# Optimization experiments

Hardware: AMD Instinct MI355X
Metric: run time of the kernel (lower is better)

Reference implementation:

```python
import jax, jax.numpy as jnp
import numpy as np

B, D, P, E = 256, 512, 128, 128  # batch, in_dim, nproto, projection_dim

def setup_inputs() -> dict:
    key = jax.random.key(0)
    k1, k2 = jax.random.split(key)
    x = jax.random.normal(k1, (B, D, P), dtype=jnp.float32)
    # glorot-uniform-like weights, one [D,E] matrix per prototype
    limit = jnp.sqrt(6.0 / (D + E)).astype(jnp.float32)
    W = jax.random.uniform(k2, (P, D, E), dtype=jnp.float32, minval=-limit, maxval=limit)
    b = jnp.zeros((P, E), dtype=jnp.float32)  # bias per prototype
    return {"x": x, "W": W, "b": b}

def reference(x, W, b):
    # Original: for each proto p, x[:,:,p] @ W_p + b_p, stacked on axis=2.
    # Fused as a single batched GEMM over the prototype axis.
    # x: [B,D,P], W: [P,D,E] -> out: [B,E,P]
    out = jnp.einsum('bdp,pde->bep', x, W)
    out = out + b.T[None, :, :]  # b: [P,E] -> broadcast [1,E,P]
    return out
```

## Files before the change

### kernel.cpp

```cpp
#include <hip/hip_runtime.h>
#include <cstdint>
#include <cstddef>

#define B_ 256
#define D_ 512
#define P_ 128
#define E_ 128

typedef unsigned short u16;
typedef unsigned int   u32;
typedef __bf16  bf16x8_t __attribute__((ext_vector_type(8)));
typedef float   f32x4_t  __attribute__((ext_vector_type(4)));
typedef u16     u16x8_t  __attribute__((ext_vector_type(8)));

__device__ __forceinline__ u16 f2bf(float f) {
  union { float f; unsigned int u; } c; c.f = f;
  unsigned int u = c.u;
  unsigned int r = (u + 0x7FFFu + ((u >> 16) & 1u)) >> 16;
  return (u16)r;
}

__global__ __launch_bounds__(256) void transpose_cvt_kernel(
    const float* __restrict__ src, u16* __restrict__ dst,
    size_t dst_row_stride, size_t dst_outer_stride) {
  __shared__ float tile[64][65];

  const int o  = blockIdx.x;
  const int r0 = blockIdx.y * 64;
  const int c0 = blockIdx.z * 64;
  const int t  = threadIdx.x;

  const float* s = src + (size_t)o * D_ * 128 + (size_t)r0 * 128 + c0;

  {
    const int lr = t >> 4;
    const int lc = (t & 15) * 4;
    #pragma unroll
    for (int it = 0; it < 4; ++it) {
      const int r = lr + it * 16;
      const float4 v = *reinterpret_cast<const float4*>(s + (size_t)r * 128 + lc);
      tile[r][lc + 0] = v.x; tile[r][lc + 1] = v.y;
      tile[r][lc + 2] = v.z; tile[r][lc + 3] = v.w;
    }
  }
  __syncthreads();

  {
    const int wc = t >> 3;
    const int wd = (t & 7) * 8;
    #pragma unroll
    for (int it = 0; it < 2; ++it) {
      const int c = wc + it * 32;
      u16x8_t pkv;
      #pragma unroll
      for (int j = 0; j < 8; ++j) pkv[j] = f2bf(tile[wd + j][c]);
      *reinterpret_cast<u16x8_t*>(dst + (size_t)(c0 + c) * dst_row_stride +
                                  (size_t)o * dst_outer_stride + r0 + wd) = pkv;
    }
  }
}


#define SWZ_ELEM(row, g) (((row) << 6) + ((((g) ^ ((row) & 7))) << 3))

__global__ __launch_bounds__(256, 4) void gemm_kernel(
    const u16* __restrict__ xT, const u16* __restrict__ Wt,
    const float* __restrict__ bias, float* __restrict__ ws2) {
  __shared__ __attribute__((aligned(16))) u16 As[2][64 * 64];
  __shared__ __attribute__((aligned(16))) u16 Bs[2][64 * 64];

  const int wg   = blockIdx.x;
  const int xcd  = wg & 7;
  const int i    = wg >> 3;
  const int p    = xcd * 16 + (i & 15);
  const int tile = i >> 4;
  const int b0   = (tile & 3) * 64;
  const int e0t  = (tile >> 2) * 64;

  const int t    = threadIdx.x;
  const int lane = t & 63;
  const int wv   = t >> 6;
  const int wr   = wv >> 1;
  const int wc   = wv & 1;

  const u16* Ag = xT + (size_t)p * (B_ * D_) + (size_t)b0 * D_;
  const u16* Bg = Wt + ((size_t)p * E_ + e0t) * D_;

  const int r1 = t >> 3;
  const int sw = (((t & 7) ^ (r1 & 7)) << 3);

  const int fr = lane & 15;
  const int fq = lane >> 4;

  f32x4_t acc[2][2] = {};

#define STAGE_AB(buf, d0) do { \
    __builtin_amdgcn_global_load_lds( \
        (const __attribute__((address_space(1))) void*)(Ag + (size_t)r1 * D_ + (d0) + sw), \
        (__attribute__((address_space(3))) void*)&As[buf][wv * 512], 16, 0, 0); \
    __builtin_amdgcn_global_load_lds( \
        (const __attribute__((address_space(1))) void*)(Ag + (size_t)(r1 + 32) * D_ + (d0) + sw), \
        (__attribute__((address_space(3))) void*)&As[buf][2048 + wv * 512], 16, 0, 0); \
    __builtin_amdgcn_global_load_lds( \
        (const __attribute__((address_space(1))) void*)(Bg + (size_t)r1 * D_ + (d0) + sw), \
        (__attribute__((address_space(3))) void*)&Bs[buf][wv * 512], 16, 0, 0); \
    __builtin_amdgcn_global_load_lds( \
        (const __attribute__((address_space(1))) void*)(Bg + (size_t)(r1 + 32) * D_ + (d0) + sw), \
        (__attribute__((address_space(3))) void*)&Bs[buf][2048 + wv * 512], 16, 0, 0); \
  } while (0)

#define MFMA(a, b, c) __builtin_amdgcn_mfma_f32_16x16x32_bf16((a), (b), (c), 0, 0, 0)

#define K_ITER(KT, PREFETCH, VMSTR, LAST) do { \
    const int rowa = wr * 32 + fr, rowb = wc * 32 + fr; \
    bf16x8_t af0 = *reinterpret_cast<const bf16x8_t*>(&As[(KT) & 1][SWZ_ELEM(rowa, fq)]); \
    bf16x8_t af1 = *reinterpret_cast<const bf16x8_t*>(&As[(KT) & 1][SWZ_ELEM(rowa, 4 + fq)]); \
    bf16x8_t af2 = *reinterpret_cast<const bf16x8_t*>(&As[(KT) & 1][SWZ_ELEM(rowa + 16, fq)]); \
    bf16x8_t af3 = *reinterpret_cast<const bf16x8_t*>(&As[(KT) & 1][SWZ_ELEM(rowa + 16, 4 + fq)]); \
    bf16x8_t bf0 = *reinterpret_cast<const bf16x8_t*>(&Bs[(KT) & 1][SWZ_ELEM(rowb, fq)]); \
    bf16x8_t bf1 = *reinterpret_cast<const bf16x8_t*>(&Bs[(KT) & 1][SWZ_ELEM(rowb, 4 + fq)]); \
    bf16x8_t bf2 = *reinterpret_cast<const bf16x8_t*>(&Bs[(KT) & 1][SWZ_ELEM(rowb + 16, fq)]); \
    bf16x8_t bf3 = *reinterpret_cast<const bf16x8_t*>(&Bs[(KT) & 1][SWZ_ELEM(rowb + 16, 4 + fq)]); \
    asm volatile("s_waitcnt lgkmcnt(0)" ::: "memory"); \
    __builtin_amdgcn_sched_barrier(0); \
    __builtin_amdgcn_s_barrier(); \
    if (PREFETCH) STAGE_AB((KT) & 1, ((KT) + 2) * 64); \
    acc[0][0] = MFMA(af0, bf0, acc[0][0]); \
    acc[0][1] = MFMA(af0, bf2, acc[0][1]); \
    acc[1][0] = MFMA(af2, bf0, acc[1][0]); \
    acc[1][1] = MFMA(af2, bf2, acc[1][1]); \
    acc[0][0] = MFMA(af1, bf1, acc[0][0]); \
    acc[0][1] = MFMA(af1, bf3, acc[0][1]); \
    acc[1][0] = MFMA(af3, bf1, acc[1][0]); \
    acc[1][1] = MFMA(af3, bf3, acc[1][1]); \
    if (!(LAST)) { \
      asm volatile("s_waitcnt " VMSTR ::: "memory"); \
      __builtin_amdgcn_sched_barrier(0); \
      __builtin_amdgcn_s_barrier(); \
    } \
  } while (0)

  STAGE_AB(0, 0);
  STAGE_AB(1, 64);
  asm volatile("s_waitcnt vmcnt(4)" ::: "memory");
  __builtin_amdgcn_sched_barrier(0);
  __builtin_amdgcn_s_barrier();

  K_ITER(0, 1, "vmcnt(4)", 0);
  K_ITER(1, 1, "vmcnt(4)", 0);
  K_ITER(2, 1, "vmcnt(4)", 0);
  K_ITER(3, 1, "vmcnt(4)", 0);
  K_ITER(4, 1, "vmcnt(4)", 0);
  K_ITER(5, 1, "vmcnt(4)", 0);
  K_ITER(6, 0, "vmcnt(0)", 0);
  K_ITER(7, 0, "vmcnt(0)", 1);

#undef K_ITER
#undef MFMA
#undef STAGE_AB

  const int q4 = fq * 4;
  #pragma unroll
  for (int jj = 0; jj < 2; ++jj) {
    const int e  = e0t + wc * 32 + jj * 16 + fr;
    const float bv = bias[p * E_ + e];
    #pragma unroll
    for (int ii = 0; ii < 2; ++ii) {
      const int r0 = b0 + wr * 32 + ii * 16 + q4;
      #pragma unroll
      for (int rg = 0; rg < 4; ++rg) {
        ws2[((size_t)p * B_ + (r0 + rg)) * E_ + e] = acc[ii][jj][rg] + bv;
      }
    }
  }
}

__global__ __launch_bounds__(256) void out_transpose_kernel(
    const float* __restrict__ ws2, float* __restrict__ out) {
  __shared__ float tile[64][65];

  const int b  = blockIdx.x;
  const int p0 = blockIdx.y * 64;
  const int e0 = blockIdx.z * 64;
  const int t  = threadIdx.x;

  const float* s = ws2 + ((size_t)p0 * B_ + b) * E_ + e0;

  {
    const int lr = t >> 4;
    const int lc = (t & 15) * 4;
    #pragma unroll
    for (int it = 0; it < 4; ++it) {
      const int r = lr + it * 16;
      const float4 v = *reinterpret_cast<const float4*>(s + (size_t)r * (B_ * E_) + lc);
      tile[r][lc + 0] = v.x; tile[r][lc + 1] = v.y;
      tile[r][lc + 2] = v.z; tile[r][lc + 3] = v.w;
    }
  }
  __syncthreads();

  {
    const int c  = t >> 4;
    const int wd = (t & 15) * 4;
    #pragma unroll
    for (int it = 0; it < 4; ++it) {
      const int cc = c + it * 16;
      float4 v;
      v.x = tile[wd + 0][cc]; v.y = tile[wd + 1][cc];
      v.z = tile[wd + 2][cc]; v.w = tile[wd + 3][cc];
      *reinterpret_cast<float4*>(out + ((size_t)b * E_ + e0 + cc) * P_ + p0 + wd) = v;
    }
  }
}

__global__ __launch_bounds__(256) void naive_kernel(
    const float* __restrict__ x, const float* __restrict__ W,
    const float* __restrict__ bias, float* __restrict__ out) {
  const size_t idx = (size_t)blockIdx.x * 256 + threadIdx.x;
  const int p = (int)(idx & 127);
  const int e = (int)((idx >> 7) & 127);
  const int b = (int)(idx >> 14);
  float acc = bias[p * E_ + e];
  const float* xp = x + (size_t)b * D_ * P_ + p;
  const float* wp = W + (size_t)p * D_ * E_ + e;
  for (int d = 0; d < D_; ++d) acc += xp[(size_t)d * P_] * wp[(size_t)d * E_];
  out[idx] = acc;
}

extern "C" void kernel_launch(void* const* d_in, const int* in_sizes, int n_in,
                              void* d_out, int out_size, void* d_ws, size_t ws_size,
                              hipStream_t stream) {
  (void)in_sizes; (void)n_in; (void)out_size;
  const float* x    = (const float*)d_in[0];
  const float* W    = (const float*)d_in[1];
  const float* bias = (const float*)d_in[2];
  float* out = (float*)d_out;

  const size_t xT_bytes  = (size_t)P_ * B_ * D_ * 2;
  const size_t Wt_bytes  = (size_t)P_ * E_ * D_ * 2;
  const size_t ws2_bytes = (size_t)P_ * B_ * E_ * 4;

  if (ws_size < xT_bytes + Wt_bytes + ws2_bytes) {
    naive_kernel<<<dim3((B_ * E_ * P_) / 256), 256, 0, stream>>>(x, W, bias, out);
    return;
  }

  u16*   xT  = (u16*)d_ws;
  u16*   Wt  = (u16*)((char*)d_ws + xT_bytes);
  float* ws2 = (float*)((char*)d_ws + xT_bytes + Wt_bytes);

  transpose_cvt_kernel<<<dim3(B_, 8, 2), 256, 0, stream>>>(
      x, xT, (size_t)B_ * D_, (size_t)D_);
  transpose_cvt_kernel<<<dim3(P_, 8, 2), 256, 0, stream>>>(
      W, Wt, (size_t)D_, (size_t)E_ * D_);

  gemm_kernel<<<dim3(1024), 256, 0, stream>>>(xT, Wt, bias, ws2);

  out_transpose_kernel<<<dim3(B_, 2, 2), 256, 0, stream>>>(ws2, out);
}
```

Baseline: 46.85 us.

## Merge input transposes, triple-buffer GEMM, store intermediate output as bf16

Combines the x and W transpose/convert kernels into one launch with a flat grid, removing a kernel launch and the gap between them. The GEMM moves from double to triple buffering in LDS with deeper prefetch, and the occupancy hint drops from 4 to 3 blocks. The GEMM result is now written as bf16 instead of fp32 and widened back in the output transpose, halving intermediate traffic. The bf16 intermediate adds rounding error to the output.

```diff
diff --git a/kernel.cpp b/kernel.cpp
--- a/kernel.cpp
+++ b/kernel.cpp
@@ -11,6 +11,7 @@
 typedef unsigned int   u32;
 typedef __bf16  bf16x8_t __attribute__((ext_vector_type(8)));
 typedef float   f32x4_t  __attribute__((ext_vector_type(4)));
+typedef u16     u16x4_t  __attribute__((ext_vector_type(4)));
 typedef u16     u16x8_t  __attribute__((ext_vector_type(8)));
 
 __device__ __forceinline__ u16 f2bf(float f) {
@@ -19,13 +20,24 @@
   unsigned int r = (u + 0x7FFFu + ((u >> 16) & 1u)) >> 16;
   return (u16)r;
 }
-
-__global__ __launch_bounds__(256) void transpose_cvt_kernel(
-    const float* __restrict__ src, u16* __restrict__ dst,
-    size_t dst_row_stride, size_t dst_outer_stride) {
+__device__ __forceinline__ float bf2f(u16 v) {
+  union { unsigned int u; float f; } c; c.u = (unsigned int)v << 16;
+  return c.f;
+}
+
+__global__ __launch_bounds__(256) void transpose_both_kernel(
+    const float* __restrict__ x, const float* __restrict__ W,
+    u16* __restrict__ xT, u16* __restrict__ Wt) {
   __shared__ float tile[64][65];
 
-  const int o  = blockIdx.x;
+  const int ob = blockIdx.x;
+  const bool isX = (ob < B_);
+  const int o = isX ? ob : (ob - B_);
+  const float* src = isX ? x : W;
+  u16* dst = isX ? xT : Wt;
+  const size_t rs = isX ? (size_t)B_ * D_ : (size_t)D_;
+  const size_t os = isX ? (size_t)D_ : (size_t)E_ * D_;
+
   const int r0 = blockIdx.y * 64;
   const int c0 = blockIdx.z * 64;
   const int t  = threadIdx.x;
@@ -54,8 +66,8 @@
       u16x8_t pkv;
       #pragma unroll
       for (int j = 0; j < 8; ++j) pkv[j] = f2bf(tile[wd + j][c]);
-      *reinterpret_cast<u16x8_t*>(dst + (size_t)(c0 + c) * dst_row_stride +
-                                  (size_t)o * dst_outer_stride + r0 + wd) = pkv;
+      *reinterpret_cast<u16x8_t*>(dst + (size_t)(c0 + c) * rs +
+                                  (size_t)o * os + r0 + wd) = pkv;
     }
   }
 }
@@ -63,11 +75,11 @@
 
 #define SWZ_ELEM(row, g) (((row) << 6) + ((((g) ^ ((row) & 7))) << 3))
 
-__global__ __launch_bounds__(256, 4) void gemm_kernel(
+__global__ __launch_bounds__(256, 3) void gemm_kernel(
     const u16* __restrict__ xT, const u16* __restrict__ Wt,
-    const float* __restrict__ bias, float* __restrict__ ws2) {
-  __shared__ __attribute__((aligned(16))) u16 As[2][64 * 64];
-  __shared__ __attribute__((aligned(16))) u16 Bs[2][64 * 64];
+    const float* __restrict__ bias, u16* __restrict__ ws2) {
+  __shared__ __attribute__((aligned(16))) u16 As[3][64 * 64];
+  __shared__ __attribute__((aligned(16))) u16 Bs[3][64 * 64];
 
   const int wg   = blockIdx.x;
   const int xcd  = wg & 7;
@@ -111,20 +123,20 @@
 
 #define MFMA(a, b, c) __builtin_amdgcn_mfma_f32_16x16x32_bf16((a), (b), (c), 0, 0, 0)
 
-#define K_ITER(KT, PREFETCH, VMSTR, LAST) do { \
+#define K_ITER(KT, BUF, PREFETCH, VMSTR, LAST) do { \
     const int rowa = wr * 32 + fr, rowb = wc * 32 + fr; \
-    bf16x8_t af0 = *reinterpret_cast<const bf16x8_t*>(&As[(KT) & 1][SWZ_ELEM(rowa, fq)]); \
-    bf16x8_t af1 = *reinterpret_cast<const bf16x8_t*>(&As[(KT) & 1][SWZ_ELEM(rowa, 4 + fq)]); \
-    bf16x8_t af2 = *reinterpret_cast<const bf16x8_t*>(&As[(KT) & 1][SWZ_ELEM(rowa + 16, fq)]); \
-    bf16x8_t af3 = *reinterpret_cast<const bf16x8_t*>(&As[(KT) & 1][SWZ_ELEM(rowa + 16, 4 + fq)]); \
-    bf16x8_t bf0 = *reinterpret_cast<const bf16x8_t*>(&Bs[(KT) & 1][SWZ_ELEM(rowb, fq)]); \
-    bf16x8_t bf1 = *reinterpret_cast<const bf16x8_t*>(&Bs[(KT) & 1][SWZ_ELEM(rowb, 4 + fq)]); \
-    bf16x8_t bf2 = *reinterpret_cast<const bf16x8_t*>(&Bs[(KT) & 1][SWZ_ELEM(rowb + 16, fq)]); \
-    bf16x8_t bf3 = *reinterpret_cast<const bf16x8_t*>(&Bs[(KT) & 1][SWZ_ELEM(rowb + 16, 4 + fq)]); \
+    bf16x8_t af0 = *reinterpret_cast<const bf16x8_t*>(&As[BUF][SWZ_ELEM(rowa, fq)]); \
+    bf16x8_t af1 = *reinterpret_cast<const bf16x8_t*>(&As[BUF][SWZ_ELEM(rowa, 4 + fq)]); \
+    bf16x8_t af2 = *reinterpret_cast<const bf16x8_t*>(&As[BUF][SWZ_ELEM(rowa + 16, fq)]); \
+    bf16x8_t af3 = *reinterpret_cast<const bf16x8_t*>(&As[BUF][SWZ_ELEM(rowa + 16, 4 + fq)]); \
+    bf16x8_t bf0 = *reinterpret_cast<const bf16x8_t*>(&Bs[BUF][SWZ_ELEM(rowb, fq)]); \
+    bf16x8_t bf1 = *reinterpret_cast<const bf16x8_t*>(&Bs[BUF][SWZ_ELEM(rowb, 4 + fq)]); \
+    bf16x8_t bf2 = *reinterpret_cast<const bf16x8_t*>(&Bs[BUF][SWZ_ELEM(rowb + 16, fq)]); \
+    bf16x8_t bf3 = *reinterpret_cast<const bf16x8_t*>(&Bs[BUF][SWZ_ELEM(rowb + 16, 4 + fq)]); \
     asm volatile("s_waitcnt lgkmcnt(0)" ::: "memory"); \
     __builtin_amdgcn_sched_barrier(0); \
     __builtin_amdgcn_s_barrier(); \
-    if (PREFETCH) STAGE_AB((KT) & 1, ((KT) + 2) * 64); \
+    if (PREFETCH) STAGE_AB(BUF, ((KT) + 3) * 64); \
     acc[0][0] = MFMA(af0, bf0, acc[0][0]); \
     acc[0][1] = MFMA(af0, bf2, acc[0][1]); \
     acc[1][0] = MFMA(af2, bf0, acc[1][0]); \
@@ -142,18 +154,19 @@
 
   STAGE_AB(0, 0);
   STAGE_AB(1, 64);
-  asm volatile("s_waitcnt vmcnt(4)" ::: "memory");
+  STAGE_AB(2, 128);
+  asm volatile("s_waitcnt vmcnt(8)" ::: "memory");
   __builtin_amdgcn_sched_barrier(0);
   __builtin_amdgcn_s_barrier();
 
-  K_ITER(0, 1, "vmcnt(4)", 0);
-  K_ITER(1, 1, "vmcnt(4)", 0);
-  K_ITER(2, 1, "vmcnt(4)", 0);
-  K_ITER(3, 1, "vmcnt(4)", 0);
-  K_ITER(4, 1, "vmcnt(4)", 0);
-  K_ITER(5, 1, "vmcnt(4)", 0);
-  K_ITER(6, 0, "vmcnt(0)", 0);
-  K_ITER(7, 0, "vmcnt(0)", 1);
+  K_ITER(0, 0, 1, "vmcnt(8)", 0);
+  K_ITER(1, 1, 1, "vmcnt(8)", 0);
+  K_ITER(2, 2, 1, "vmcnt(8)", 0);
+  K_ITER(3, 0, 1, "vmcnt(8)", 0);
+  K_ITER(4, 1, 1, "vmcnt(8)", 0);
+  K_ITER(5, 2, 0, "vmcnt(4)", 0);
+  K_ITER(6, 0, 0, "vmcnt(0)", 0);
+  K_ITER(7, 1, 0, "vmcnt(0)", 1);
 
 #undef K_ITER
 #undef MFMA
@@ -169,14 +182,14 @@
       const int r0 = b0 + wr * 32 + ii * 16 + q4;
       #pragma unroll
       for (int rg = 0; rg < 4; ++rg) {
-        ws2[((size_t)p * B_ + (r0 + rg)) * E_ + e] = acc[ii][jj][rg] + bv;
+        ws2[((size_t)p * B_ + (r0 + rg)) * E_ + e] = f2bf(acc[ii][jj][rg] + bv);
       }
     }
   }
 }
 
 __global__ __launch_bounds__(256) void out_transpose_kernel(
-    const float* __restrict__ ws2, float* __restrict__ out) {
+    const u16* __restrict__ ws2, float* __restrict__ out) {
   __shared__ float tile[64][65];
 
   const int b  = blockIdx.x;
@@ -184,7 +197,7 @@
   const int e0 = blockIdx.z * 64;
   const int t  = threadIdx.x;
 
-  const float* s = ws2 + ((size_t)p0 * B_ + b) * E_ + e0;
+  const u16* s = ws2 + ((size_t)p0 * B_ + b) * E_ + e0;
 
   {
     const int lr = t >> 4;
@@ -192,9 +205,9 @@
     #pragma unroll
     for (int it = 0; it < 4; ++it) {
       const int r = lr + it * 16;
-      const float4 v = *reinterpret_cast<const float4*>(s + (size_t)r * (B_ * E_) + lc);
-      tile[r][lc + 0] = v.x; tile[r][lc + 1] = v.y;
-      tile[r][lc + 2] = v.z; tile[r][lc + 3] = v.w;
+      const u16x4_t v = *reinterpret_cast<const u16x4_t*>(s + (size_t)r * (B_ * E_) + lc);
+      tile[r][lc + 0] = bf2f(v[0]); tile[r][lc + 1] = bf2f(v[1]);
+      tile[r][lc + 2] = bf2f(v[2]); tile[r][lc + 3] = bf2f(v[3]);
     }
   }
   __syncthreads();
@@ -238,23 +251,18 @@
 
   const size_t xT_bytes  = (size_t)P_ * B_ * D_ * 2;
   const size_t Wt_bytes  = (size_t)P_ * E_ * D_ * 2;
-  const size_t ws2_bytes = (size_t)P_ * B_ * E_ * 4;
+  const size_t ws2_bytes = (size_t)P_ * B_ * E_ * 2;
 
   if (ws_size < xT_bytes + Wt_bytes + ws2_bytes) {
     naive_kernel<<<dim3((B_ * E_ * P_) / 256), 256, 0, stream>>>(x, W, bias, out);
     return;
   }
 
-  u16*   xT  = (u16*)d_ws;
-  u16*   Wt  = (u16*)((char*)d_ws + xT_bytes);
-  float* ws2 = (float*)((char*)d_ws + xT_bytes + Wt_bytes);
-
-  transpose_cvt_kernel<<<dim3(B_, 8, 2), 256, 0, stream>>>(
-      x, xT, (size_t)B_ * D_, (size_t)D_);
-  transpose_cvt_kernel<<<dim3(P_, 8, 2), 256, 0, stream>>>(
-      W, Wt, (size_t)D_, (size_t)E_ * D_);
-
+  u16* xT  = (u16*)d_ws;
+  u16* Wt  = (u16*)((char*)d_ws + xT_bytes);
+  u16* ws2 = (u16*)((char*)d_ws + xT_bytes + Wt_bytes);
+
+  transpose_both_kernel<<<dim3(B_ + P_, 8, 2), 256, 0, stream>>>(x, W, xT, Wt);
   gemm_kernel<<<dim3(1024), 256, 0, stream>>>(xT, Wt, bias, ws2);
-
   out_transpose_kernel<<<dim3(B_, 2, 2), 256, 0, stream>>>(ws2, out);
 }
```

After: 47.75 us. About the same (+1.9%).
